# Optimization experiments

Hardware: AMD Instinct MI355X
Metric: run time of the kernel (lower is better)

The kernel has to match this reference:

```python
import jax, jax.numpy as jnp
import numpy as np

N, E = 50000, 800000
DIM_IN, DIM_H, DIM_OUT, HEADS = 128, 32, 16, 4
HID = DIM_H * HEADS  # 128
FINAL = DIM_OUT * HEADS  # 64
NEG_SLOPE = 0.2


def _glorot(key, shape):
    fan_in, fan_out = shape[0], shape[-1] if len(shape) > 1 else shape[0]
    lim = jnp.sqrt(6.0 / (fan_in + fan_out)).astype(jnp.float32)
    return jax.random.uniform(key, shape, jnp.float32, -lim, lim)


def setup_inputs() -> dict:
    key = jax.random.key(0)
    ks = jax.random.split(key, 16)
    x = jax.random.normal(ks[0], (N, DIM_IN), jnp.float32)
    edge_index = jax.random.randint(ks[1], (2, E), 0, N, dtype=jnp.int64)
    inp = {"x": x, "edge_index": edge_index}
    # layer 1: DIM_IN -> HEADS*DIM_H
    inp["Wl1"] = _glorot(ks[2], (DIM_IN, HEADS * DIM_H))
    inp["Wr1"] = _glorot(ks[3], (DIM_IN, HEADS * DIM_H))
    inp["att1"] = _glorot(ks[4], (HEADS, DIM_H))
    inp["b1"] = jnp.zeros((HEADS * DIM_H,), jnp.float32)
    # layer 2: HID -> HEADS*DIM_H
    inp["Wl2"] = _glorot(ks[5], (HID, HEADS * DIM_H))
    inp["Wr2"] = _glorot(ks[6], (HID, HEADS * DIM_H))
    inp["att2"] = _glorot(ks[7], (HEADS, DIM_H))
    inp["b2"] = jnp.zeros((HEADS * DIM_H,), jnp.float32)
    # layer 3: HID -> HEADS*DIM_OUT
    inp["Wl3"] = _glorot(ks[8], (HID, HEADS * DIM_OUT))
    inp["Wr3"] = _glorot(ks[9], (HID, HEADS * DIM_OUT))
    inp["att3"] = _glorot(ks[10], (HEADS, DIM_OUT))
    inp["b3"] = jnp.zeros((HEADS * DIM_OUT,), jnp.float32)
    return inp


def gatv2_conv(x, src, dst, Wl, Wr, att, b, heads, ch):
    n = x.shape[0]
    xl = (x @ Wl).reshape(n, heads, ch)  # source-side transform
    xr = (x @ Wr).reshape(n, heads, ch)  # target-side transform
    m = xl[src] + xr[dst]                 # [E, H, C]
    e = jnp.einsum('ehc,hc->eh', jax.nn.leaky_relu(m, NEG_SLOPE), att)
    # segment softmax over incoming edges of each dst node
    emax = jax.ops.segment_max(e, dst, num_segments=n)
    ex = jnp.exp(e - emax[dst])
    denom = jax.ops.segment_sum(ex, dst, num_segments=n)
    alpha = ex / denom[dst]               # [E, H]
    out = jax.ops.segment_sum(alpha[:, :, None] * xl[src], dst, num_segments=n)
    return out.reshape(n, heads * ch) + b


def reference(x, edge_index, Wl1, Wr1, att1, b1, Wl2, Wr2, att2, b2, Wl3, Wr3, att3, b3):
    n = x.shape[0]
    loops = jnp.arange(n, dtype=edge_index.dtype)
    src = jnp.concatenate([edge_index[0], loops])  # PyG add_self_loops=True
    dst = jnp.concatenate([edge_index[1], loops])
    # dropout is identity in eval mode
    h = jax.nn.elu(gatv2_conv(x, src, dst, Wl1, Wr1, att1, b1, HEADS, DIM_H))
    h = jax.nn.elu(gatv2_conv(h, src, dst, Wl2, Wr2, att2, b2, HEADS, DIM_H))
    h = gatv2_conv(h, src, dst, Wl3, Wr3, att3, b3, HEADS, DIM_OUT)
    return jax.nn.log_softmax(h, axis=1)
```

## Files before the change

kernel.cpp:

```cpp
#include <hip/hip_runtime.h>
#include <math.h>

constexpr int DIN  = 128;
constexpr int FSH  = 8;
constexpr int NFBM = 200;
constexpr int LCAP = 72;
constexpr int RND  = 4096;
constexpr int FCAP = 4608;

typedef __attribute__((ext_vector_type(8))) short short8;
typedef __attribute__((ext_vector_type(4))) float f32x4;

__device__ __forceinline__ unsigned short f2bf(float f) {
  unsigned u = __float_as_uint(f);
  u = (u + 0x7FFF + ((u >> 16) & 1)) >> 16;
  return (unsigned short)u;
}
__device__ __forceinline__ float bflo(unsigned u) { return __uint_as_float(u << 16); }
__device__ __forceinline__ float bfhi(unsigned u) { return __uint_as_float(u & 0xFFFF0000u); }

__device__ __forceinline__ void unpack8(uint4 u, float* x) {
  x[0] = bflo(u.x); x[1] = bfhi(u.x); x[2] = bflo(u.y); x[3] = bfhi(u.y);
  x[4] = bflo(u.z); x[5] = bfhi(u.z); x[6] = bflo(u.w); x[7] = bfhi(u.w);
}
__device__ __forceinline__ void unpack4(uint2 u, float* x) {
  x[0] = bflo(u.x); x[1] = bfhi(u.x); x[2] = bflo(u.y); x[3] = bfhi(u.y);
}

typedef const __attribute__((address_space(1))) unsigned int guint_t;
typedef __attribute__((address_space(3))) unsigned int luint_t;
__device__ __forceinline__ void async16(const void* g, void* l) {
  __builtin_amdgcn_global_load_lds((guint_t*)g, (luint_t*)l, 16, 0, 0);
}


__global__ __launch_bounds__(256) void bucket_append_kernel(const int* __restrict__ ei,
    int* __restrict__ gcnt, unsigned* __restrict__ gpairs, int E, int nfb) {
  __shared__ unsigned buf[NFBM * LCAP];
  __shared__ int cnt[NFBM];
  __shared__ int gbase[NFBM];
  const int tid = threadIdx.x;
  if (tid < NFBM) cnt[tid] = 0;
  __syncthreads();

  const int k0 = blockIdx.x * RND;
  for (int i = tid; i < RND; i += 256) {
    int k = k0 + i;
    if (k >= E) break;
    int src = ei[k], dst = ei[E + k];
    int fb = dst >> FSH;
    int pos = atomicAdd(&cnt[fb], 1);
    if (pos < LCAP)
      buf[fb * LCAP + pos] = (unsigned)src | ((unsigned)(dst & ((1 << FSH) - 1)) << 16);
  }
  __syncthreads();

  if (tid < nfb) gbase[tid] = atomicAdd(&gcnt[tid], min(cnt[tid], LCAP));
  __syncthreads();

  const int wid = tid >> 6, lane = tid & 63;
  for (int fb = wid; fb < nfb; fb += 4) {
    int c  = min(cnt[fb], LCAP);
    int gb = gbase[fb];
    if (gb >= FCAP) continue;
    c = min(c, FCAP - gb);
    unsigned* dstp = gpairs + (size_t)fb * FCAP + gb;
    const unsigned* srcp = &buf[fb * LCAP];
    for (int i = lane; i < c; i += 64) dstp[i] = srcp[i];
  }
}

__global__ __launch_bounds__(256) void bucket_build_kernel(const unsigned* __restrict__ gpairs,
    const int* __restrict__ gcnt, int* __restrict__ row_ptr,
    unsigned short* __restrict__ edge_src, int n, int nfb) {
  const int b   = blockIdx.x;
  const int tid = threadIdx.x;
  const int lane = tid & 63, wid = tid >> 6;
  __shared__ int hist[1 << FSH];
  __shared__ int wsum[4];
  __shared__ int base_s;

  const int d0 = b << FSH;
  const int nvalid = min(1 << FSH, n - d0);

  if (wid == 0) {
    int term = 0;
    for (int i = lane; i < b; i += 64)
      term += min(gcnt[i], FCAP) + min(1 << FSH, n - (i << FSH));
#pragma unroll
    for (int o = 32; o >= 1; o >>= 1) term += __shfl_xor(term, o, 64);
    if (lane == 0) base_s = term;
  }
  hist[tid] = (tid < nvalid) ? 1 : 0;
  __syncthreads();

  const int cnt = min(gcnt[b], FCAP);
  const unsigned* bp = gpairs + (size_t)b * FCAP;
  for (int i = tid; i < cnt; i += 256)
    atomicAdd(&hist[bp[i] >> 16], 1);
  __syncthreads();

  const int h = hist[tid];
  int incl = h;
#pragma unroll
  for (int o = 1; o < 64; o <<= 1) {
    int t = __shfl_up(incl, o, 64);
    if (lane >= o) incl += t;
  }
  if (lane == 63) wsum[wid] = incl;
  __syncthreads();
  int wo = 0;
  for (int wq = 0; wq < wid; ++wq) wo += wsum[wq];
  const int base = base_s;
  const int excl = wo + incl - h;
  if (tid < nvalid) {
    row_ptr[d0 + tid] = base + excl;
    edge_src[base + excl] = (unsigned short)(d0 + tid);
    hist[tid] = excl + 1;
  } else if (d0 + tid == n) {
    row_ptr[n] = base + excl;
  }
  if (b == nfb - 1 && d0 + (1 << FSH) <= n && tid == 0)
    row_ptr[n] = base + cnt + nvalid;
  __syncthreads();

  for (int i = tid; i < cnt; i += 256) {
    unsigned p = bp[i];
    int pos = atomicAdd(&hist[p >> 16], 1);
    edge_src[base + pos] = (unsigned short)(p & 0xFFFFu);
  }
}

__global__ __launch_bounds__(256) void cvt_w_kernel(
    const float* __restrict__ Wl1, const float* __restrict__ Wr1,
    const float* __restrict__ Wl2, const float* __restrict__ Wr2,
    const float* __restrict__ Wl3, const float* __restrict__ Wr3,
    unsigned short* __restrict__ Wt, int* __restrict__ gcnt) {
  if (blockIdx.x == 0 && threadIdx.x < NFBM) gcnt[threadIdx.x] = 0;
  int e = blockIdx.x * 256 + threadIdx.x;
  if (e >= 81920) return;
  const float* src; int N; int off;
  if (e < 65536) {
    int m = e >> 14; off = e & 16383; N = 128;
    src = (m == 0) ? Wl1 : (m == 1) ? Wr1 : (m == 2) ? Wl2 : Wr2;
  } else {
    int e2 = e - 65536; int m = e2 >> 13; off = e2 & 8191; N = 64;
    src = m ? Wr3 : Wl3;
  }
  int nn = off >> 7, k = off & 127;
  Wt[e] = f2bf(src[(size_t)k * N + nn]);
}


template<int NC, bool CVT>
__global__ __launch_bounds__(256) void gemm2_mfma(const void* __restrict__ Ap,
    const unsigned short* __restrict__ Wlt, const unsigned short* __restrict__ Wrt,
    unsigned short* __restrict__ outl, unsigned short* __restrict__ outr, int M) {
  constexpr int WNB = NC / 16;
  __shared__ char lds[16384 + NC * 256];
  char* As = lds;
  char* Ws = lds + 16384;
  const int tid  = threadIdx.x;
  const int w    = tid >> 6, lane = tid & 63;
  const int q    = lane >> 4, r15 = lane & 15;
  const int row0 = blockIdx.x * 64;

  if constexpr (CVT) {
    const float* Af = (const float*)Ap;
    for (int idx = tid * 4; idx < 64 * 128; idx += 1024) {
      int rl = idx >> 7, k = idx & 127;
      int rg = row0 + rl; if (rg >= M) rg = M - 1;
      float4 v = *(const float4*)&Af[(size_t)rg * 128 + k];
      uint2 pk;
      pk.x = (unsigned)f2bf(v.x) | ((unsigned)f2bf(v.y) << 16);
      pk.y = (unsigned)f2bf(v.z) | ((unsigned)f2bf(v.w) << 16);
      char* addr = As + (rl >> 4) * 4096 + (k >> 5) * 1024 +
                   ((((k >> 3) & 3) * 16) + (rl & 15)) * 16 + (k & 7) * 2;
      *(uint2*)addr = pk;
    }
  } else {
    const unsigned short* A = (const unsigned short*)Ap;
    int r = row0 + w * 16 + r15; if (r >= M) r = M - 1;
    const char* g = (const char*)A + (size_t)r * 256 + q * 16;
    char* l = As + w * 4096;
#pragma unroll
    for (int kk = 0; kk < 4; ++kk) async16(g + kk * 64, l + kk * 1024);
  }
  for (int nt = w; nt < WNB; nt += 4) {
    const char* g = (const char*)Wlt + ((size_t)(nt * 16 + r15)) * 256 + q * 16;
    char* l = Ws + nt * 4096;
#pragma unroll
    for (int kk = 0; kk < 4; ++kk) async16(g + kk * 64, l + kk * 1024);
  }
  __syncthreads();

  const char* aw = As + w * 4096;
  f32x4 acc[WNB] = {};
#pragma unroll
  for (int kk = 0; kk < 4; ++kk) {
    short8 af = *(const short8*)(aw + kk * 1024 + (size_t)lane * 16);
#pragma unroll
    for (int nt = 0; nt < WNB; ++nt) {
      short8 bf = *(const short8*)(Ws + (nt * 4 + kk) * 1024 + (size_t)lane * 16);
      acc[nt] = __builtin_amdgcn_mfma_f32_16x16x32_bf16(af, bf, acc[nt], 0, 0, 0);
    }
  }
  {
    int rowb = row0 + w * 16 + q * 4;
#pragma unroll
    for (int nt = 0; nt < WNB; ++nt)
#pragma unroll
      for (int r = 0; r < 4; ++r) {
        int rr = rowb + r;
        if (rr < M) outl[(size_t)rr * NC + nt * 16 + r15] = f2bf(acc[nt][r]);
      }
  }
  __syncthreads();
  for (int nt = w; nt < WNB; nt += 4) {
    const char* g = (const char*)Wrt + ((size_t)(nt * 16 + r15)) * 256 + q * 16;
    char* l = Ws + nt * 4096;
#pragma unroll
    for (int kk = 0; kk < 4; ++kk) async16(g + kk * 64, l + kk * 1024);
  }
  __syncthreads();

  f32x4 acc2[WNB] = {};
#pragma unroll
  for (int kk = 0; kk < 4; ++kk) {
    short8 af = *(const short8*)(aw + kk * 1024 + (size_t)lane * 16);
#pragma unroll
    for (int nt = 0; nt < WNB; ++nt) {
      short8 bf = *(const short8*)(Ws + (nt * 4 + kk) * 1024 + (size_t)lane * 16);
      acc2[nt] = __builtin_amdgcn_mfma_f32_16x16x32_bf16(af, bf, acc2[nt], 0, 0, 0);
    }
  }
  {
    int rowb = row0 + w * 16 + q * 4;
#pragma unroll
    for (int nt = 0; nt < WNB; ++nt)
#pragma unroll
      for (int r = 0; r < 4; ++r) {
        int rr = rowb + r;
        if (rr < M) outr[(size_t)rr * NC + nt * 16 + r15] = f2bf(acc2[nt][r]);
      }
  }
}


__global__ __launch_bounds__(256) void aggregate128_kernel(
    const unsigned short* __restrict__ xl, const unsigned short* __restrict__ xr,
    const float* __restrict__ att, const float* __restrict__ bias,
    const int* __restrict__ row_ptr, const unsigned short* __restrict__ edge_src,
    unsigned short* __restrict__ out, int n) {
  const int tid  = threadIdx.x;
  const int r    = tid & 15;
  const int node = blockIdx.x * 16 + (tid >> 4);
  if (node >= n) return;
  const int c0 = r * 8;

  float xrv[8];
  unpack8(*(const uint4*)&xr[(size_t)node * 128 + c0], xrv);
  float a6[8], a4[8];
  {
    float4 aa = *(const float4*)&att[c0];
    float4 ab = *(const float4*)&att[c0 + 4];
    float at[8] = {aa.x, aa.y, aa.z, aa.w, ab.x, ab.y, ab.z, ab.w};
#pragma unroll
    for (int j = 0; j < 8; ++j) { a6[j] = 0.6f * at[j]; a4[j] = 0.4f * at[j]; }
  }

  float l = 0.f, o[8] = {};
  int idx = row_ptr[node];
  const int end = row_ptr[node + 1];

  int s0 = 0, s1 = 0, s2 = 0, s3 = 0;
  if (idx + 4 <= end) {
    s0 = edge_src[idx];     s1 = edge_src[idx + 1];
    s2 = edge_src[idx + 2]; s3 = edge_src[idx + 3];
  }
  while (idx + 4 <= end) {
    uint4 u0 = *(const uint4*)&xl[(size_t)s0 * 128 + c0];
    uint4 u1 = *(const uint4*)&xl[(size_t)s1 * 128 + c0];
    uint4 u2 = *(const uint4*)&xl[(size_t)s2 * 128 + c0];
    uint4 u3 = *(const uint4*)&xl[(size_t)s3 * 128 + c0];
    idx += 4;
    if (idx + 4 <= end) {
      s0 = edge_src[idx];     s1 = edge_src[idx + 1];
      s2 = edge_src[idx + 2]; s3 = edge_src[idx + 3];
    }
    float x0[8], x1[8], x2[8], x3[8];
    unpack8(u0, x0); unpack8(u1, x1); unpack8(u2, x2); unpack8(u3, x3);
    float p0 = 0.f, p1 = 0.f, p2 = 0.f, p3 = 0.f;
#pragma unroll
    for (int j = 0; j < 8; ++j) {
      float t0 = x0[j] + xrv[j], t1 = x1[j] + xrv[j];
      float t2 = x2[j] + xrv[j], t3 = x3[j] + xrv[j];
      p0 = fmaf(t0, a6[j], p0); p0 = fmaf(fabsf(t0), a4[j], p0);
      p1 = fmaf(t1, a6[j], p1); p1 = fmaf(fabsf(t1), a4[j], p1);
      p2 = fmaf(t2, a6[j], p2); p2 = fmaf(fabsf(t2), a4[j], p2);
      p3 = fmaf(t3, a6[j], p3); p3 = fmaf(fabsf(t3), a4[j], p3);
    }
    p0 += __shfl_xor(p0, 1, 64); p0 += __shfl_xor(p0, 2, 64);
    p1 += __shfl_xor(p1, 1, 64); p1 += __shfl_xor(p1, 2, 64);
    p2 += __shfl_xor(p2, 1, 64); p2 += __shfl_xor(p2, 2, 64);
    p3 += __shfl_xor(p3, 1, 64); p3 += __shfl_xor(p3, 2, 64);
    float e0 = __expf(fminf(p0, 80.f)), e1 = __expf(fminf(p1, 80.f));
    float e2 = __expf(fminf(p2, 80.f)), e3 = __expf(fminf(p3, 80.f));
    l += (e0 + e1) + (e2 + e3);
#pragma unroll
    for (int j = 0; j < 8; ++j)
      o[j] = fmaf(e0, x0[j], fmaf(e1, x1[j], fmaf(e2, x2[j], fmaf(e3, x3[j], o[j]))));
  }
  for (; idx < end; ++idx) {
    int s = edge_src[idx];
    uint4 u0 = *(const uint4*)&xl[(size_t)s * 128 + c0];
    float x0[8];
    unpack8(u0, x0);
    float p0 = 0.f;
#pragma unroll
    for (int j = 0; j < 8; ++j) {
      float t = x0[j] + xrv[j];
      p0 = fmaf(t, a6[j], p0); p0 = fmaf(fabsf(t), a4[j], p0);
    }
    p0 += __shfl_xor(p0, 1, 64); p0 += __shfl_xor(p0, 2, 64);
    float e0 = __expf(fminf(p0, 80.f));
    l += e0;
#pragma unroll
    for (int j = 0; j < 8; ++j) o[j] = fmaf(e0, x0[j], o[j]);
  }

  float4 b0 = *(const float4*)&bias[c0];
  float4 b1 = *(const float4*)&bias[c0 + 4];
  float bb[8] = {b0.x, b0.y, b0.z, b0.w, b1.x, b1.y, b1.z, b1.w};
  float rl = 1.f / l;
  unsigned short res[8];
#pragma unroll
  for (int j = 0; j < 8; ++j) {
    float v = o[j] * rl + bb[j];
    v = v > 0.f ? v : __expf(v) - 1.f;
    res[j] = f2bf(v);
  }
  uint4 ov;
  ov.x = (unsigned)res[0] | ((unsigned)res[1] << 16);
  ov.y = (unsigned)res[2] | ((unsigned)res[3] << 16);
  ov.z = (unsigned)res[4] | ((unsigned)res[5] << 16);
  ov.w = (unsigned)res[6] | ((unsigned)res[7] << 16);
  *(uint4*)&out[(size_t)node * 128 + c0] = ov;
}


__global__ __launch_bounds__(256) void aggregate64_kernel(
    const unsigned short* __restrict__ xl, const unsigned short* __restrict__ xr,
    const float* __restrict__ att, const float* __restrict__ bias,
    const int* __restrict__ row_ptr, const unsigned short* __restrict__ edge_src,
    float* __restrict__ out, int n) {
  const int tid  = threadIdx.x;
  const int r    = tid & 15;
  const int node = blockIdx.x * 16 + (tid >> 4);
  if (node >= n) return;
  const int c0 = r * 4;

  float xrv[4];
  unpack4(*(const uint2*)&xr[(size_t)node * 64 + c0], xrv);
  float a6[4], a4[4];
  {
    float4 aa = *(const float4*)&att[c0];
    float at[4] = {aa.x, aa.y, aa.z, aa.w};
#pragma unroll
    for (int j = 0; j < 4; ++j) { a6[j] = 0.6f * at[j]; a4[j] = 0.4f * at[j]; }
  }

  float l = 0.f, o[4] = {};
  int idx = row_ptr[node];
  const int end = row_ptr[node + 1];

  int s0 = 0, s1 = 0, s2 = 0, s3 = 0;
  if (idx + 4 <= end) {
    s0 = edge_src[idx];     s1 = edge_src[idx + 1];
    s2 = edge_src[idx + 2]; s3 = edge_src[idx + 3];
  }
  while (idx + 4 <= end) {
    uint2 u0 = *(const uint2*)&xl[(size_t)s0 * 64 + c0];
    uint2 u1 = *(const uint2*)&xl[(size_t)s1 * 64 + c0];
    uint2 u2 = *(const uint2*)&xl[(size_t)s2 * 64 + c0];
    uint2 u3 = *(const uint2*)&xl[(size_t)s3 * 64 + c0];
    idx += 4;
    if (idx + 4 <= end) {
      s0 = edge_src[idx];     s1 = edge_src[idx + 1];
      s2 = edge_src[idx + 2]; s3 = edge_src[idx + 3];
    }
    float x0[4], x1[4], x2[4], x3[4];
    unpack4(u0, x0); unpack4(u1, x1); unpack4(u2, x2); unpack4(u3, x3);
    float p0 = 0.f, p1 = 0.f, p2 = 0.f, p3 = 0.f;
#pragma unroll
    for (int j = 0; j < 4; ++j) {
      float t0 = x0[j] + xrv[j], t1 = x1[j] + xrv[j];
      float t2 = x2[j] + xrv[j], t3 = x3[j] + xrv[j];
      p0 = fmaf(t0, a6[j], p0); p0 = fmaf(fabsf(t0), a4[j], p0);
      p1 = fmaf(t1, a6[j], p1); p1 = fmaf(fabsf(t1), a4[j], p1);
      p2 = fmaf(t2, a6[j], p2); p2 = fmaf(fabsf(t2), a4[j], p2);
      p3 = fmaf(t3, a6[j], p3); p3 = fmaf(fabsf(t3), a4[j], p3);
    }
    p0 += __shfl_xor(p0, 1, 64); p0 += __shfl_xor(p0, 2, 64);
    p1 += __shfl_xor(p1, 1, 64); p1 += __shfl_xor(p1, 2, 64);
    p2 += __shfl_xor(p2, 1, 64); p2 += __shfl_xor(p2, 2, 64);
    p3 += __shfl_xor(p3, 1, 64); p3 += __shfl_xor(p3, 2, 64);
    float e0 = __expf(fminf(p0, 80.f)), e1 = __expf(fminf(p1, 80.f));
    float e2 = __expf(fminf(p2, 80.f)), e3 = __expf(fminf(p3, 80.f));
    l += (e0 + e1) + (e2 + e3);
#pragma unroll
    for (int j = 0; j < 4; ++j)
      o[j] = fmaf(e0, x0[j], fmaf(e1, x1[j], fmaf(e2, x2[j], fmaf(e3, x3[j], o[j]))));
  }
  for (; idx < end; ++idx) {
    int s = edge_src[idx];
    uint2 u0 = *(const uint2*)&xl[(size_t)s * 64 + c0];
    float x0[4];
    unpack4(u0, x0);
    float p0 = 0.f;
#pragma unroll
    for (int j = 0; j < 4; ++j) {
      float t = x0[j] + xrv[j];
      p0 = fmaf(t, a6[j], p0); p0 = fmaf(fabsf(t), a4[j], p0);
    }
    p0 += __shfl_xor(p0, 1, 64); p0 += __shfl_xor(p0, 2, 64);
    float e0 = __expf(fminf(p0, 80.f));
    l += e0;
#pragma unroll
    for (int j = 0; j < 4; ++j) o[j] = fmaf(e0, x0[j], o[j]);
  }

  float4 bv = *(const float4*)&bias[c0];
  float bb[4] = {bv.x, bv.y, bv.z, bv.w};
  float rl = 1.f / l;
  float rr[4];
#pragma unroll
  for (int j = 0; j < 4; ++j) rr[j] = o[j] * rl + bb[j];

  float mx = fmaxf(fmaxf(rr[0], rr[1]), fmaxf(rr[2], rr[3]));
#pragma unroll
  for (int off = 1; off < 16; off <<= 1) mx = fmaxf(mx, __shfl_xor(mx, off, 64));
  float se = __expf(rr[0] - mx) + __expf(rr[1] - mx) +
             __expf(rr[2] - mx) + __expf(rr[3] - mx);
#pragma unroll
  for (int off = 1; off < 16; off <<= 1) se += __shfl_xor(se, off, 64);
  float ls = mx + __logf(se);
  *(float4*)&out[(size_t)node * 64 + c0] =
      make_float4(rr[0] - ls, rr[1] - ls, rr[2] - ls, rr[3] - ls);
}


extern "C" void kernel_launch(void* const* d_in, const int* in_sizes, int n_in,
                              void* d_out, int out_size, void* d_ws, size_t ws_size,
                              hipStream_t stream) {
  const float* x    = (const float*)d_in[0];
  const int*   ei   = (const int*)d_in[1];
  const float* Wl1  = (const float*)d_in[2];
  const float* Wr1  = (const float*)d_in[3];
  const float* att1 = (const float*)d_in[4];
  const float* b1   = (const float*)d_in[5];
  const float* Wl2  = (const float*)d_in[6];
  const float* Wr2  = (const float*)d_in[7];
  const float* att2 = (const float*)d_in[8];
  const float* b2   = (const float*)d_in[9];
  const float* Wl3  = (const float*)d_in[10];
  const float* Wr3  = (const float*)d_in[11];
  const float* att3 = (const float*)d_in[12];
  const float* b3   = (const float*)d_in[13];
  const int n = in_sizes[0] / DIN;
  const int E = in_sizes[1] / 2;
  float* out = (float*)d_out;

  const int nfb = (n + (1 << FSH) - 1) >> FSH;

  unsigned short* xl = (unsigned short*)d_ws;
  unsigned short* xr = xl + (size_t)n * 128;
  unsigned short* h  = xr + (size_t)n * 128;
  unsigned short* Wt = h + (size_t)n * 128;
  unsigned short* Wl1t = Wt, *Wr1t = Wt + 16384;
  unsigned short* Wl2t = Wt + 32768, *Wr2t = Wt + 49152;
  unsigned short* Wl3t = Wt + 65536, *Wr3t = Wt + 73728;
  int* row_ptr  = (int*)(Wt + 81920);
  int* gcnt     = row_ptr + (n + 16);
  unsigned short* edge_src = (unsigned short*)(gcnt + NFBM);
  unsigned* gpairs = (unsigned*)((char*)edge_src +
      ((((size_t)(E + n) * 2) + 15) & ~(size_t)15));

  cvt_w_kernel<<<320, 256, 0, stream>>>(Wl1, Wr1, Wl2, Wr2, Wl3, Wr3, Wt, gcnt);

  bucket_append_kernel<<<(E + RND - 1) / RND, 256, 0, stream>>>(ei, gcnt, gpairs, E, nfb);
  bucket_build_kernel<<<nfb, 256, 0, stream>>>(gpairs, gcnt, row_ptr, edge_src, n, nfb);

  const int gb = (n + 63) / 64;
  const int ab = (n + 15) / 16;

  gemm2_mfma<128, true><<<gb, 256, 0, stream>>>(x, Wl1t, Wr1t, xl, xr, n);
  aggregate128_kernel<<<ab, 256, 0, stream>>>(xl, xr, att1, b1, row_ptr, edge_src, h, n);
  gemm2_mfma<128, false><<<gb, 256, 0, stream>>>(h, Wl2t, Wr2t, xl, xr, n);
  aggregate128_kernel<<<ab, 256, 0, stream>>>(xl, xr, att2, b2, row_ptr, edge_src, h, n);
  gemm2_mfma<64, false><<<gb, 256, 0, stream>>>(h, Wl3t, Wr3t, xl, xr, n);
  aggregate64_kernel<<<ab, 256, 0, stream>>>(xl, xr, att3, b3, row_ptr, edge_src, out, n);
}
```

Before: 275.5 us.

## Merge independent preprocessing kernels to cut launch count

Weight conversion now runs as extra blocks inside the bucket-append kernel, and the CSR bucket-build blocks share a launch with the first-layer GEMM blocks through a shared-memory union. The gcnt reset moves to a hipMemsetAsync. This removes two kernel launches and their serialization gaps, because the fused pieces are independent and can overlap. In exchange, the build blocks occupy GEMM-sized LDS allocations, and a memset node is added.

```diff
diff --git a/kernel.cpp b/kernel.cpp
--- a/kernel.cpp
+++ b/kernel.cpp
@@ -34,12 +34,33 @@
 }
 
 
-__global__ __launch_bounds__(256) void bucket_append_kernel(const int* __restrict__ ei,
-    int* __restrict__ gcnt, unsigned* __restrict__ gpairs, int E, int nfb) {
+__global__ __launch_bounds__(256) void prep_kernel(const int* __restrict__ ei,
+    int* __restrict__ gcnt, unsigned* __restrict__ gpairs, int E, int nfb, int appb,
+    const float* __restrict__ Wl1, const float* __restrict__ Wr1,
+    const float* __restrict__ Wl2, const float* __restrict__ Wr2,
+    const float* __restrict__ Wl3, const float* __restrict__ Wr3,
+    unsigned short* __restrict__ Wt) {
   __shared__ unsigned buf[NFBM * LCAP];
   __shared__ int cnt[NFBM];
   __shared__ int gbase[NFBM];
   const int tid = threadIdx.x;
+
+  if (blockIdx.x >= appb) {
+    int e = (blockIdx.x - appb) * 256 + tid;
+    if (e >= 81920) return;
+    const float* src; int N; int off;
+    if (e < 65536) {
+      int m = e >> 14; off = e & 16383; N = 128;
+      src = (m == 0) ? Wl1 : (m == 1) ? Wr1 : (m == 2) ? Wl2 : Wr2;
+    } else {
+      int e2 = e - 65536; int m = e2 >> 13; off = e2 & 8191; N = 64;
+      src = m ? Wr3 : Wl3;
+    }
+    int nn = off >> 7, k = off & 127;
+    Wt[e] = f2bf(src[(size_t)k * N + nn]);
+    return;
+  }
+
   if (tid < NFBM) cnt[tid] = 0;
   __syncthreads();
 
@@ -70,15 +91,15 @@
   }
 }
 
-__global__ __launch_bounds__(256) void bucket_build_kernel(const unsigned* __restrict__ gpairs,
-    const int* __restrict__ gcnt, int* __restrict__ row_ptr,
-    unsigned short* __restrict__ edge_src, int n, int nfb) {
-  const int b   = blockIdx.x;
+
+struct BuildSmem { int hist[1 << FSH]; int wsum[4]; int base_s; };
+
+__device__ __forceinline__ void build_body(BuildSmem& s, int b,
+    const unsigned* __restrict__ gpairs, const int* __restrict__ gcnt,
+    int* __restrict__ row_ptr, unsigned short* __restrict__ edge_src,
+    int n, int nfb) {
   const int tid = threadIdx.x;
   const int lane = tid & 63, wid = tid >> 6;
-  __shared__ int hist[1 << FSH];
-  __shared__ int wsum[4];
-  __shared__ int base_s;
 
   const int d0 = b << FSH;
   const int nvalid = min(1 << FSH, n - d0);
@@ -89,34 +110,34 @@
       term += min(gcnt[i], FCAP) + min(1 << FSH, n - (i << FSH));
 #pragma unroll
     for (int o = 32; o >= 1; o >>= 1) term += __shfl_xor(term, o, 64);
-    if (lane == 0) base_s = term;
-  }
-  hist[tid] = (tid < nvalid) ? 1 : 0;
+    if (lane == 0) s.base_s = term;
+  }
+  s.hist[tid] = (tid < nvalid) ? 1 : 0;
   __syncthreads();
 
   const int cnt = min(gcnt[b], FCAP);
   const unsigned* bp = gpairs + (size_t)b * FCAP;
   for (int i = tid; i < cnt; i += 256)
-    atomicAdd(&hist[bp[i] >> 16], 1);
-  __syncthreads();
-
-  const int h = hist[tid];
+    atomicAdd(&s.hist[bp[i] >> 16], 1);
+  __syncthreads();
+
+  const int h = s.hist[tid];
   int incl = h;
 #pragma unroll
   for (int o = 1; o < 64; o <<= 1) {
     int t = __shfl_up(incl, o, 64);
     if (lane >= o) incl += t;
   }
-  if (lane == 63) wsum[wid] = incl;
+  if (lane == 63) s.wsum[wid] = incl;
   __syncthreads();
   int wo = 0;
-  for (int wq = 0; wq < wid; ++wq) wo += wsum[wq];
-  const int base = base_s;
+  for (int wq = 0; wq < wid; ++wq) wo += s.wsum[wq];
+  const int base = s.base_s;
   const int excl = wo + incl - h;
   if (tid < nvalid) {
     row_ptr[d0 + tid] = base + excl;
     edge_src[base + excl] = (unsigned short)(d0 + tid);
-    hist[tid] = excl + 1;
+    s.hist[tid] = excl + 1;
   } else if (d0 + tid == n) {
     row_ptr[n] = base + excl;
   }
@@ -126,44 +147,23 @@
 
   for (int i = tid; i < cnt; i += 256) {
     unsigned p = bp[i];
-    int pos = atomicAdd(&hist[p >> 16], 1);
+    int pos = atomicAdd(&s.hist[p >> 16], 1);
     edge_src[base + pos] = (unsigned short)(p & 0xFFFFu);
   }
 }
 
-__global__ __launch_bounds__(256) void cvt_w_kernel(
-    const float* __restrict__ Wl1, const float* __restrict__ Wr1,
-    const float* __restrict__ Wl2, const float* __restrict__ Wr2,
-    const float* __restrict__ Wl3, const float* __restrict__ Wr3,
-    unsigned short* __restrict__ Wt, int* __restrict__ gcnt) {
-  if (blockIdx.x == 0 && threadIdx.x < NFBM) gcnt[threadIdx.x] = 0;
-  int e = blockIdx.x * 256 + threadIdx.x;
-  if (e >= 81920) return;
-  const float* src; int N; int off;
-  if (e < 65536) {
-    int m = e >> 14; off = e & 16383; N = 128;
-    src = (m == 0) ? Wl1 : (m == 1) ? Wr1 : (m == 2) ? Wl2 : Wr2;
-  } else {
-    int e2 = e - 65536; int m = e2 >> 13; off = e2 & 8191; N = 64;
-    src = m ? Wr3 : Wl3;
-  }
-  int nn = off >> 7, k = off & 127;
-  Wt[e] = f2bf(src[(size_t)k * N + nn]);
-}
-
 
 template<int NC, bool CVT>
-__global__ __launch_bounds__(256) void gemm2_mfma(const void* __restrict__ Ap,
+__device__ __forceinline__ void gemm2_body(char* lds, int bid, const void* __restrict__ Ap,
     const unsigned short* __restrict__ Wlt, const unsigned short* __restrict__ Wrt,
     unsigned short* __restrict__ outl, unsigned short* __restrict__ outr, int M) {
   constexpr int WNB = NC / 16;
-  __shared__ char lds[16384 + NC * 256];
   char* As = lds;
   char* Ws = lds + 16384;
   const int tid  = threadIdx.x;
   const int w    = tid >> 6, lane = tid & 63;
   const int q    = lane >> 4, r15 = lane & 15;
-  const int row0 = blockIdx.x * 64;
+  const int row0 = bid * 64;
 
   if constexpr (CVT) {
     const float* Af = (const float*)Ap;
@@ -244,6 +244,30 @@
         if (rr < M) outr[(size_t)rr * NC + nt * 16 + r15] = f2bf(acc2[nt][r]);
       }
   }
+}
+
+template<int NC, bool CVT>
+__global__ __launch_bounds__(256) void gemm2_mfma(const void* __restrict__ Ap,
+    const unsigned short* __restrict__ Wlt, const unsigned short* __restrict__ Wrt,
+    unsigned short* __restrict__ outl, unsigned short* __restrict__ outr, int M) {
+  __shared__ char lds[16384 + NC * 256];
+  gemm2_body<NC, CVT>(lds, blockIdx.x, Ap, Wlt, Wrt, outl, outr, M);
+}
+
+
+union GemmBuildSmem { char lds[16384 + 128 * 256]; BuildSmem b; };
+
+__global__ __launch_bounds__(256) void gemm1_build_kernel(const void* __restrict__ Ap,
+    const unsigned short* __restrict__ Wlt, const unsigned short* __restrict__ Wrt,
+    unsigned short* __restrict__ outl, unsigned short* __restrict__ outr,
+    const unsigned* __restrict__ gpairs, const int* __restrict__ gcnt,
+    int* __restrict__ row_ptr, unsigned short* __restrict__ edge_src,
+    int n, int nfb) {
+  __shared__ GemmBuildSmem smem;
+  if (blockIdx.x < (unsigned)nfb)
+    build_body(smem.b, blockIdx.x, gpairs, gcnt, row_ptr, edge_src, n, nfb);
+  else
+    gemm2_body<128, true>(smem.lds, blockIdx.x - nfb, Ap, Wlt, Wrt, outl, outr, n);
 }
 
 
@@ -471,7 +495,8 @@
   const int E = in_sizes[1] / 2;
   float* out = (float*)d_out;
 
-  const int nfb = (n + (1 << FSH) - 1) >> FSH;
+  const int nfb  = (n + (1 << FSH) - 1) >> FSH;
+  const int appb = (E + RND - 1) / RND;
 
   unsigned short* xl = (unsigned short*)d_ws;
   unsigned short* xr = xl + (size_t)n * 128;
@@ -486,15 +511,17 @@
   unsigned* gpairs = (unsigned*)((char*)edge_src +
       ((((size_t)(E + n) * 2) + 15) & ~(size_t)15));
 
-  cvt_w_kernel<<<320, 256, 0, stream>>>(Wl1, Wr1, Wl2, Wr2, Wl3, Wr3, Wt, gcnt);
-
-  bucket_append_kernel<<<(E + RND - 1) / RND, 256, 0, stream>>>(ei, gcnt, gpairs, E, nfb);
-  bucket_build_kernel<<<nfb, 256, 0, stream>>>(gpairs, gcnt, row_ptr, edge_src, n, nfb);
+  hipMemsetAsync(gcnt, 0, NFBM * sizeof(int), stream);
+
+  prep_kernel<<<appb + 320, 256, 0, stream>>>(ei, gcnt, gpairs, E, nfb, appb,
+                                              Wl1, Wr1, Wl2, Wr2, Wl3, Wr3, Wt);
 
   const int gb = (n + 63) / 64;
   const int ab = (n + 15) / 16;
 
-  gemm2_mfma<128, true><<<gb, 256, 0, stream>>>(x, Wl1t, Wr1t, xl, xr, n);
+  gemm1_build_kernel<<<nfb + gb, 256, 0, stream>>>(x, Wl1t, Wr1t, xl, xr,
+                                                   gpairs, gcnt, row_ptr, edge_src, n, nfb);
+
   aggregate128_kernel<<<ab, 256, 0, stream>>>(xl, xr, att1, b1, row_ptr, edge_src, h, n);
   gemm2_mfma<128, false><<<gb, 256, 0, stream>>>(h, Wl2t, Wr2t, xl, xr, n);
   aggregate128_kernel<<<ab, 256, 0, stream>>>(xl, xr, att2, b2, row_ptr, edge_src, h, n);
```

New measurement: 265.5 us. 3.6% less time.
